# Kernel tuning notes

Measured on AMD Instinct MI355X. Metric: run time of the kernel, lower is better.

Reference implementation:

```python
import jax, jax.numpy as jnp
import numpy as np

D_MODEL = 1024
N_HEADS = 16
D_K = D_MODEL // N_HEADS


def setup_inputs() -> dict:
    key = jax.random.key(0)
    ks = jax.random.split(key, 10)
    B, L = 2, 2048
    s = 1.0 / np.sqrt(D_MODEL)
    inp = {
        "x": jax.random.normal(ks[0], (B, L, D_MODEL), dtype=jnp.float32),
        "bond_influence": jax.random.uniform(ks[1], (B, L, L), dtype=jnp.float32),
        "Wq": jax.random.uniform(ks[2], (D_MODEL, D_MODEL), jnp.float32, -s, s),
        "bq": jax.random.uniform(ks[3], (D_MODEL,), jnp.float32, -s, s),
        "Wk": jax.random.uniform(ks[4], (D_MODEL, D_MODEL), jnp.float32, -s, s),
        "bk": jax.random.uniform(ks[5], (D_MODEL,), jnp.float32, -s, s),
        "Wv": jax.random.uniform(ks[6], (D_MODEL, D_MODEL), jnp.float32, -s, s),
        "bv": jax.random.uniform(ks[7], (D_MODEL,), jnp.float32, -s, s),
        "Wo": jax.random.uniform(ks[8], (D_MODEL, D_MODEL), jnp.float32, -s, s),
        "bo": jax.random.uniform(ks[9], (D_MODEL,), jnp.float32, -s, s),
    }
    return inp


def reference(x, bond_influence, Wq, bq, Wk, bk, Wv, bv, Wo, bo):
    B, L, _ = x.shape
    # QKV projections -> [B, H, L, d_k]
    def proj(W, b):
        return (x @ W + b).reshape(B, L, N_HEADS, D_K).transpose(0, 2, 1, 3)
    Q = proj(Wq, bq)
    K = proj(Wk, bk)
    V = proj(Wv, bv)
    # scores: [B, H, L, L], scaled then modulated by per-batch bond influence
    scores = jnp.einsum('bhqd,bhkd->bhqk', Q, K) / jnp.sqrt(jnp.float32(D_K))
    scores = scores * bond_influence[:, None, :, :]
    attn = jax.nn.softmax(scores, axis=-1)
    out = jnp.einsum('bhqk,bhkd->bhqd', attn, V)  # [B, H, L, d_k]
    out = out.transpose(0, 2, 1, 3).reshape(B, L, D_MODEL)
    return out @ Wo + bo
```

## Files before the change

### kernel.cpp

```cpp
#include <hip/hip_runtime.h>
#include <stdint.h>

typedef unsigned short u16;
typedef __attribute__((ext_vector_type(8))) short bf16x8;
typedef __attribute__((ext_vector_type(4))) float f32x4;

__device__ __forceinline__ u16 f2bf(float f) {
    union { float f; uint32_t u; } v; v.f = f;
    uint32_t u = v.u + 0x7fffu + ((v.u >> 16) & 1u);
    return (u16)(u >> 16);
}
__device__ __forceinline__ float bf2f(u16 s) {
    union { uint32_t u; float f; } v; v.u = ((uint32_t)s) << 16;
    return v.f;
}
__device__ __forceinline__ uint32_t packbf(float a, float b) {
    union { float f; uint32_t u; } ua, ub; ua.f = a; ub.f = b;
    return ((ua.u + 0x8000u) >> 16) | ((ub.u + 0x8000u) & 0xffff0000u);
}

__device__ __forceinline__ void gld16(const void* g, void* l) {
    __builtin_amdgcn_global_load_lds((const __attribute__((address_space(1))) void*)g,
                                     (__attribute__((address_space(3))) void*)l,
                                     16, 0, 0);
}


__global__ void cvt_bf16_kernel(const float* __restrict__ s, u16* __restrict__ d, int n4) {
    int i = blockIdx.x * blockDim.x + threadIdx.x;
    const int stride = gridDim.x * blockDim.x;
    for (; i < n4; i += stride) {
        float4 v = ((const float4*)s)[i];
        ushort4 o;
        o.x = f2bf(v.x); o.y = f2bf(v.y); o.z = f2bf(v.z); o.w = f2bf(v.w);
        ((ushort4*)d)[i] = o;
    }
}

__global__ void transpose_bf16_kernel(const float* __restrict__ src, u16* __restrict__ dst) {
    __shared__ float tile[32][33];
    const int tx = threadIdx.x, ty = threadIdx.y;
    const int bx = blockIdx.x * 32, by = blockIdx.y * 32;
#pragma unroll
    for (int i = ty; i < 32; i += 8)
        tile[i][tx] = src[(size_t)(by + i) * 1024 + bx + tx];
    __syncthreads();
#pragma unroll
    for (int i = ty; i < 32; i += 8)
        dst[(size_t)(bx + i) * 1024 + by + tx] = f2bf(tile[tx][i]);
}


template <int EPI>
__global__ __launch_bounds__(256) void gemm128(
    const u16* __restrict__ A, const u16* __restrict__ Bt,
    const float* __restrict__ bias0, const float* __restrict__ bias1,
    const float* __restrict__ bias2,
    u16* __restrict__ o_q, u16* __restrict__ o_k, u16* __restrict__ o_vt,
    float* __restrict__ o_f)
{
    constexpr int K = 1024;
    __shared__ u16 As[128 * 32];
    __shared__ u16 Bs[128 * 32];
    const int t = threadIdx.x;
    const int lane = t & 63, w = t >> 6;
    const int wm = w >> 1, wn = w & 1;
    const int g = lane >> 4, r = lane & 15;
    const int mbase = blockIdx.y * 128, nbase = blockIdx.x * 128;

    const f32x4 zero4 = {0.f, 0.f, 0.f, 0.f};
    f32x4 acc[4][4];
#pragma unroll
    for (int m = 0; m < 4; ++m)
#pragma unroll
        for (int n = 0; n < 4; ++n) acc[m][n] = zero4;

    for (int k0 = 0; k0 < K; k0 += 32) {
#pragma unroll
        for (int i = 0; i < 2; ++i) {
            const int base = i * 256 + (w << 6);
            const int idx = base + lane;
            const int row = idx >> 2, cc = (idx & 3) << 3;
            gld16(A + (size_t)(mbase + row) * K + k0 + cc, (char*)As + base * 16);
            gld16(Bt + (size_t)(nbase + row) * K + k0 + cc, (char*)Bs + base * 16);
        }
        __syncthreads();

        bf16x8 af[4], bfr[4];
#pragma unroll
        for (int m = 0; m < 4; ++m)
            af[m] = *(const bf16x8*)&As[(wm * 64 + m * 16 + r) * 32 + g * 8];
#pragma unroll
        for (int n = 0; n < 4; ++n)
            bfr[n] = *(const bf16x8*)&Bs[(wn * 64 + n * 16 + r) * 32 + g * 8];
        __builtin_amdgcn_s_setprio(1);
#pragma unroll
        for (int m = 0; m < 4; ++m)
#pragma unroll
            for (int n = 0; n < 4; ++n)
                acc[m][n] = __builtin_amdgcn_mfma_f32_16x16x32_bf16(af[m], bfr[n], acc[m][n], 0, 0, 0);
        __builtin_amdgcn_s_setprio(0);
        __syncthreads();
    }

#pragma unroll
    for (int m = 0; m < 4; ++m) {
#pragma unroll
        for (int n = 0; n < 4; ++n) {
            const int c = nbase + wn * 64 + n * 16 + r;
#pragma unroll
            for (int j = 0; j < 4; ++j) {
                const int rr = mbase + wm * 64 + m * 16 + g * 4 + j;
                const float y = acc[m][n][j];
                if (EPI == 0) {
                    const int which = c >> 10, d = c & 1023;
                    const int b = rr >> 11, l = rr & 2047;
                    const int h = d >> 6, dd = d & 63;
                    const size_t bh = (size_t)(b * 16 + h);
                    if (which == 0) {
                        o_q[(bh * 2048 + l) * 64 + dd] = f2bf((y + bias0[d]) * 0.125f);
                    } else if (which == 1) {
                        o_k[(bh * 2048 + l) * 64 + dd] = f2bf(y + bias1[d]);
                    } else {
                        o_vt[(bh * 64 + dd) * 2048 + l] = f2bf(y + bias2[d]);
                    }
                } else {
                    o_f[(size_t)rr * 1024 + c] = y + bias0[c];
                }
            }
        }
    }
}


__global__ __launch_bounds__(128, 2) void attn_kernel(
    const u16* __restrict__ qb, const u16* __restrict__ kb,
    const u16* __restrict__ vtb, const float* __restrict__ bondf,
    u16* __restrict__ attnout)
{
    __shared__ u16 Ks[2][64 * 64];
    __shared__ u16 Vs[2][64 * 64];
    __shared__ u16 Ps[2][32 * 64];
    const int t = threadIdx.x;
    const int lane = t & 63, w = t >> 6;
    const int g = lane >> 4, r = lane & 15;
    const int sw = r & 7;
    const int flat = blockIdx.x;
    const int wg = (flat & 7) * 128 + (flat >> 3);
    const int bh = wg >> 5, qt = wg & 31;
    const int b = bh >> 4, h = bh & 15;
    const int q0 = qt * 64 + w * 32;
    const size_t kvBase = (size_t)bh * 2048 * 64;
    const size_t bondRow0 = ((size_t)b * 2048 + q0 + r) * 2048;

    bf16x8 aq[2][2];
#pragma unroll
    for (int qf = 0; qf < 2; ++qf)
#pragma unroll
        for (int kz = 0; kz < 2; ++kz)
            aq[qf][kz] = *(const bf16x8*)&qb[kvBase + (size_t)(q0 + qf * 16 + r) * 64 + kz * 32 + g * 8];

    const f32x4 zero4 = {0.f, 0.f, 0.f, 0.f};
    f32x4 o[2][4];
#pragma unroll
    for (int qf = 0; qf < 2; ++qf)
#pragma unroll
        for (int nf = 0; nf < 4; ++nf) o[qf][nf] = zero4;
    float sm[2] = {0.f, 0.f};

#pragma unroll
    for (int i = 0; i < 4; ++i) {
        const int idx = i * 128 + t;
        const int row = idx >> 3, ch = idx & 7;
        const int chg = ch ^ (row & 7);
        gld16(kb + kvBase + (size_t)row * 64 + chg * 8, (char*)&Ks[0][0] + idx * 16);
        gld16(vtb + ((size_t)bh * 64 + row) * 2048 + chg * 8, (char*)&Vs[0][0] + idx * 16);
    }
    float4 bd[2][4], bdn[2][4];
#pragma unroll
    for (int qf = 0; qf < 2; ++qf)
#pragma unroll
        for (int kf = 0; kf < 4; ++kf)
            bd[qf][kf] = *(const float4*)&bondf[bondRow0 + (size_t)qf * 16 * 2048 + kf * 16 + g * 4];
    __syncthreads();

    for (int it = 0; it < 32; ++it) {
        const int cur = it & 1;
        const int kt = it * 64;
        if (it < 31) {
            const int kt2 = kt + 64;
#pragma unroll
            for (int i = 0; i < 4; ++i) {
                const int idx = i * 128 + t;
                const int row = idx >> 3, ch = idx & 7;
                const int chg = ch ^ (row & 7);
                gld16(kb + kvBase + (size_t)(kt2 + row) * 64 + chg * 8, (char*)&Ks[cur ^ 1][0] + idx * 16);
                gld16(vtb + ((size_t)bh * 64 + row) * 2048 + kt2 + chg * 8, (char*)&Vs[cur ^ 1][0] + idx * 16);
            }
#pragma unroll
            for (int qf = 0; qf < 2; ++qf)
#pragma unroll
                for (int kf = 0; kf < 4; ++kf)
                    bdn[qf][kf] = *(const float4*)&bondf[bondRow0 + (size_t)qf * 16 * 2048 + kt2 + kf * 16 + g * 4];
        }

        f32x4 st[2][4];
#pragma unroll
        for (int qf = 0; qf < 2; ++qf)
#pragma unroll
            for (int kf = 0; kf < 4; ++kf) st[qf][kf] = zero4;
        {
            bf16x8 kfr[2][2];
#pragma unroll
            for (int kz = 0; kz < 2; ++kz)
#pragma unroll
                for (int kf = 0; kf < 2; ++kf)
                    kfr[kz][kf] = *(const bf16x8*)((const char*)&Ks[cur][0] +
                                    (kf * 16 + r) * 128 + (((kz * 4 + g) ^ sw) * 16));
            __builtin_amdgcn_s_setprio(1);
#pragma unroll
            for (int kz = 0; kz < 2; ++kz)
#pragma unroll
                for (int qf = 0; qf < 2; ++qf)
#pragma unroll
                    for (int kf = 0; kf < 2; ++kf)
                        st[qf][kf] = __builtin_amdgcn_mfma_f32_16x16x32_bf16(kfr[kz][kf], aq[qf][kz], st[qf][kf], 0, 0, 0);
            __builtin_amdgcn_s_setprio(0);
        }

#pragma unroll
        for (int qf = 0; qf < 2; ++qf)
#pragma unroll
            for (int kf = 0; kf < 2; ++kf) {
                const float p0 = __expf(st[qf][kf][0] * bd[qf][kf].x);
                const float p1 = __expf(st[qf][kf][1] * bd[qf][kf].y);
                const float p2 = __expf(st[qf][kf][2] * bd[qf][kf].z);
                const float p3 = __expf(st[qf][kf][3] * bd[qf][kf].w);
                sm[qf] += (p0 + p1) + (p2 + p3);
                uint2 pk;
                pk.x = packbf(p0, p1);
                pk.y = packbf(p2, p3);
                *(uint2*)((char*)&Ps[w][0] + (qf * 16 + r) * 128 + ((kf * 32 + g * 8) ^ (sw << 4))) = pk;
            }

        {
            bf16x8 kfr[2][2];
#pragma unroll
            for (int kz = 0; kz < 2; ++kz)
#pragma unroll
                for (int kf = 0; kf < 2; ++kf)
                    kfr[kz][kf] = *(const bf16x8*)((const char*)&Ks[cur][0] +
                                    ((kf + 2) * 16 + r) * 128 + (((kz * 4 + g) ^ sw) * 16));
            __builtin_amdgcn_s_setprio(1);
#pragma unroll
            for (int kz = 0; kz < 2; ++kz)
#pragma unroll
                for (int qf = 0; qf < 2; ++qf)
#pragma unroll
                    for (int kf = 0; kf < 2; ++kf)
                        st[qf][kf + 2] = __builtin_amdgcn_mfma_f32_16x16x32_bf16(kfr[kz][kf], aq[qf][kz], st[qf][kf + 2], 0, 0, 0);
            __builtin_amdgcn_s_setprio(0);
        }

        {
            bf16x8 ap[2], bv_[4];
#pragma unroll
            for (int qf = 0; qf < 2; ++qf)
                ap[qf] = *(const bf16x8*)((const char*)&Ps[w][0] +
                            (qf * 16 + r) * 128 + ((g * 16) ^ (sw << 4)));
#pragma unroll
            for (int nf = 0; nf < 4; ++nf)
                bv_[nf] = *(const bf16x8*)((const char*)&Vs[cur][0] +
                            (nf * 16 + r) * 128 + ((g ^ sw) * 16));
            __builtin_amdgcn_s_setprio(1);
#pragma unroll
            for (int qf = 0; qf < 2; ++qf)
#pragma unroll
                for (int nf = 0; nf < 4; ++nf)
                    o[qf][nf] = __builtin_amdgcn_mfma_f32_16x16x32_bf16(ap[qf], bv_[nf], o[qf][nf], 0, 0, 0);
            __builtin_amdgcn_s_setprio(0);
        }

#pragma unroll
        for (int qf = 0; qf < 2; ++qf)
#pragma unroll
            for (int kf = 2; kf < 4; ++kf) {
                const float p0 = __expf(st[qf][kf][0] * bd[qf][kf].x);
                const float p1 = __expf(st[qf][kf][1] * bd[qf][kf].y);
                const float p2 = __expf(st[qf][kf][2] * bd[qf][kf].z);
                const float p3 = __expf(st[qf][kf][3] * bd[qf][kf].w);
                sm[qf] += (p0 + p1) + (p2 + p3);
                uint2 pk;
                pk.x = packbf(p0, p1);
                pk.y = packbf(p2, p3);
                *(uint2*)((char*)&Ps[w][0] + (qf * 16 + r) * 128 + ((kf * 32 + g * 8) ^ (sw << 4))) = pk;
            }

        {
            bf16x8 ap[2], bv_[4];
#pragma unroll
            for (int qf = 0; qf < 2; ++qf)
                ap[qf] = *(const bf16x8*)((const char*)&Ps[w][0] +
                            (qf * 16 + r) * 128 + ((64 + g * 16) ^ (sw << 4)));
#pragma unroll
            for (int nf = 0; nf < 4; ++nf)
                bv_[nf] = *(const bf16x8*)((const char*)&Vs[cur][0] +
                            (nf * 16 + r) * 128 + (((4 + g) ^ sw) * 16));
            __builtin_amdgcn_s_setprio(1);
#pragma unroll
            for (int qf = 0; qf < 2; ++qf)
#pragma unroll
                for (int nf = 0; nf < 4; ++nf)
                    o[qf][nf] = __builtin_amdgcn_mfma_f32_16x16x32_bf16(ap[qf], bv_[nf], o[qf][nf], 0, 0, 0);
            __builtin_amdgcn_s_setprio(0);
        }

        if (it < 31) {
#pragma unroll
            for (int qf = 0; qf < 2; ++qf)
#pragma unroll
                for (int kf = 0; kf < 4; ++kf)
                    bd[qf][kf] = bdn[qf][kf];
        }
        __syncthreads();
    }

#pragma unroll
    for (int qf = 0; qf < 2; ++qf) {
        sm[qf] += __shfl_xor(sm[qf], 16, 64);
        sm[qf] += __shfl_xor(sm[qf], 32, 64);
    }
    float* Lw = (float*)&Ps[w][0];
    if (g == 0) { Lw[r] = sm[0]; Lw[16 + r] = sm[1]; }
    __syncthreads();
    f32x4 lv[2];
    lv[0] = *(const f32x4*)&Lw[g * 4];
    lv[1] = *(const f32x4*)&Lw[16 + g * 4];

#pragma unroll
    for (int qf = 0; qf < 2; ++qf)
#pragma unroll
        for (int j = 0; j < 4; ++j) {
            const float inv = 1.f / lv[qf][j];
            const size_t orow = ((size_t)b * 2048 + q0 + qf * 16 + g * 4 + j) * 1024 + h * 64;
#pragma unroll
            for (int nf = 0; nf < 4; ++nf)
                attnout[orow + nf * 16 + r] = f2bf(o[qf][nf][j] * inv);
        }
}


extern "C" void kernel_launch(void* const* d_in, const int* in_sizes, int n_in,
                              void* d_out, int out_size, void* d_ws, size_t ws_size,
                              hipStream_t stream) {
    (void)in_sizes; (void)n_in; (void)out_size; (void)ws_size;
    const float* x    = (const float*)d_in[0];
    const float* bond = (const float*)d_in[1];
    const float* Wq   = (const float*)d_in[2];
    const float* bq   = (const float*)d_in[3];
    const float* Wk   = (const float*)d_in[4];
    const float* bk   = (const float*)d_in[5];
    const float* Wv   = (const float*)d_in[6];
    const float* bv   = (const float*)d_in[7];
    const float* Wo   = (const float*)d_in[8];
    const float* bo   = (const float*)d_in[9];
    float* out = (float*)d_out;

    char* ws = (char*)d_ws;
    u16* xb      = (u16*)(ws);
    u16* wqkvt   = (u16*)(ws + 8388608);
    u16* wot     = (u16*)(ws + 14680064);
    u16* qb      = (u16*)(ws + 16777216);
    u16* kb_     = (u16*)(ws + 25165824);
    u16* vtb     = (u16*)(ws + 33554432);
    u16* attnout = (u16*)(ws + 58720256);

    dim3 tb(32, 8);
    transpose_bf16_kernel<<<dim3(32, 32), tb, 0, stream>>>(Wq, wqkvt);
    transpose_bf16_kernel<<<dim3(32, 32), tb, 0, stream>>>(Wk, wqkvt + 1024 * 1024);
    transpose_bf16_kernel<<<dim3(32, 32), tb, 0, stream>>>(Wv, wqkvt + 2 * 1024 * 1024);
    transpose_bf16_kernel<<<dim3(32, 32), tb, 0, stream>>>(Wo, wot);
    cvt_bf16_kernel<<<1024, 256, 0, stream>>>(x, xb, 4194304 / 4);

    gemm128<0><<<dim3(24, 32), 256, 0, stream>>>(xb, wqkvt, bq, bk, bv, qb, kb_, vtb, nullptr);
    attn_kernel<<<dim3(1024), 128, 0, stream>>>(qb, kb_, vtb, bond, attnout);
    gemm128<1><<<dim3(8, 32), 256, 0, stream>>>(attnout, wot, bo, nullptr, nullptr,
                                                nullptr, nullptr, nullptr, out);
}
```

Baseline: 171.8 us.

## Keep softmax probabilities in registers via permlane swap instead of LDS round-trip

The attention kernel no longer writes the exponentiated scores to shared memory and reads them back as MFMA A-operands. It repacks them in registers with v_permlane16_swap and permutes the V fragment reads to match the new k ordering. The row-sum broadcast now uses a warp shuffle instead of an LDS write plus __syncthreads. The four weight-transpose launches are also merged into one 3D-grid launch. This cuts LDS traffic, a barrier and launch overhead, but relies on the gfx950 permlane instruction and on the permuted V indexing being correct.

```diff
diff --git a/kernel.cpp b/kernel.cpp
--- a/kernel.cpp
+++ b/kernel.cpp
@@ -10,10 +10,6 @@
     uint32_t u = v.u + 0x7fffu + ((v.u >> 16) & 1u);
     return (u16)(u >> 16);
 }
-__device__ __forceinline__ float bf2f(u16 s) {
-    union { uint32_t u; float f; } v; v.u = ((uint32_t)s) << 16;
-    return v.f;
-}
 __device__ __forceinline__ uint32_t packbf(float a, float b) {
     union { float f; uint32_t u; } ua, ub; ua.f = a; ub.f = b;
     return ((ua.u + 0x8000u) >> 16) | ((ub.u + 0x8000u) & 0xffff0000u);
@@ -23,6 +19,10 @@
     __builtin_amdgcn_global_load_lds((const __attribute__((address_space(1))) void*)g,
                                      (__attribute__((address_space(3))) void*)l,
                                      16, 0, 0);
+}
+
+__device__ __forceinline__ void plswap16(uint32_t& a, uint32_t& b) {
+    asm volatile("v_permlane16_swap_b32 %0, %1" : "+v"(a), "+v"(b));
 }
 
 
@@ -37,8 +37,13 @@
     }
 }
 
-__global__ void transpose_bf16_kernel(const float* __restrict__ src, u16* __restrict__ dst) {
+__global__ void transpose4_bf16_kernel(const float* __restrict__ Wq, const float* __restrict__ Wk,
+                                       const float* __restrict__ Wv, const float* __restrict__ Wo,
+                                       u16* __restrict__ dqkv, u16* __restrict__ dо) {
     __shared__ float tile[32][33];
+    const int z = blockIdx.z;
+    const float* src = (z == 0) ? Wq : (z == 1) ? Wk : (z == 2) ? Wv : Wo;
+    u16* dst = (z < 3) ? (dqkv + (size_t)z * 1024 * 1024) : dо;
     const int tx = threadIdx.x, ty = threadIdx.y;
     const int bx = blockIdx.x * 32, by = blockIdx.y * 32;
 #pragma unroll
@@ -140,11 +145,11 @@
 {
     __shared__ u16 Ks[2][64 * 64];
     __shared__ u16 Vs[2][64 * 64];
-    __shared__ u16 Ps[2][32 * 64];
     const int t = threadIdx.x;
     const int lane = t & 63, w = t >> 6;
     const int g = lane >> 4, r = lane & 15;
     const int sw = r & 7;
+    const int pg = ((g & 1) << 1) | (g >> 1);
     const int flat = blockIdx.x;
     const int wg = (flat & 7) * 128 + (flat >> 3);
     const int bh = wg >> 5, qt = wg & 31;
@@ -205,10 +210,6 @@
         }
 
         f32x4 st[2][4];
-#pragma unroll
-        for (int qf = 0; qf < 2; ++qf)
-#pragma unroll
-            for (int kf = 0; kf < 4; ++kf) st[qf][kf] = zero4;
         {
             bf16x8 kfr[2][2];
 #pragma unroll
@@ -217,6 +218,10 @@
                 for (int kf = 0; kf < 2; ++kf)
                     kfr[kz][kf] = *(const bf16x8*)((const char*)&Ks[cur][0] +
                                     (kf * 16 + r) * 128 + (((kz * 4 + g) ^ sw) * 16));
+#pragma unroll
+            for (int qf = 0; qf < 2; ++qf)
+#pragma unroll
+                for (int kf = 0; kf < 2; ++kf) st[qf][kf] = zero4;
             __builtin_amdgcn_s_setprio(1);
 #pragma unroll
             for (int kz = 0; kz < 2; ++kz)
@@ -228,8 +233,10 @@
             __builtin_amdgcn_s_setprio(0);
         }
 
-#pragma unroll
-        for (int qf = 0; qf < 2; ++qf)
+        bf16x8 ap0[2], ap1[2];
+#pragma unroll
+        for (int qf = 0; qf < 2; ++qf) {
+            uint32_t pkl[2], pkh[2];
 #pragma unroll
             for (int kf = 0; kf < 2; ++kf) {
                 const float p0 = __expf(st[qf][kf][0] * bd[qf][kf].x);
@@ -237,11 +244,15 @@
                 const float p2 = __expf(st[qf][kf][2] * bd[qf][kf].z);
                 const float p3 = __expf(st[qf][kf][3] * bd[qf][kf].w);
                 sm[qf] += (p0 + p1) + (p2 + p3);
-                uint2 pk;
-                pk.x = packbf(p0, p1);
-                pk.y = packbf(p2, p3);
-                *(uint2*)((char*)&Ps[w][0] + (qf * 16 + r) * 128 + ((kf * 32 + g * 8) ^ (sw << 4))) = pk;
+                pkl[kf] = packbf(p0, p1);
+                pkh[kf] = packbf(p2, p3);
             }
+            plswap16(pkl[0], pkl[1]);
+            plswap16(pkh[0], pkh[1]);
+            union { uint32_t u[4]; bf16x8 v; } a;
+            a.u[0] = pkl[0]; a.u[1] = pkh[0]; a.u[2] = pkl[1]; a.u[3] = pkh[1];
+            ap0[qf] = a.v;
+        }
 
         {
             bf16x8 kfr[2][2];
@@ -251,6 +262,10 @@
                 for (int kf = 0; kf < 2; ++kf)
                     kfr[kz][kf] = *(const bf16x8*)((const char*)&Ks[cur][0] +
                                     ((kf + 2) * 16 + r) * 128 + (((kz * 4 + g) ^ sw) * 16));
+#pragma unroll
+            for (int qf = 0; qf < 2; ++qf)
+#pragma unroll
+                for (int kf = 0; kf < 2; ++kf) st[qf][kf + 2] = zero4;
             __builtin_amdgcn_s_setprio(1);
 #pragma unroll
             for (int kz = 0; kz < 2; ++kz)
@@ -263,55 +278,52 @@
         }
 
         {
-            bf16x8 ap[2], bv_[4];
-#pragma unroll
-            for (int qf = 0; qf < 2; ++qf)
-                ap[qf] = *(const bf16x8*)((const char*)&Ps[w][0] +
-                            (qf * 16 + r) * 128 + ((g * 16) ^ (sw << 4)));
+            bf16x8 bv_[4];
 #pragma unroll
             for (int nf = 0; nf < 4; ++nf)
                 bv_[nf] = *(const bf16x8*)((const char*)&Vs[cur][0] +
-                            (nf * 16 + r) * 128 + ((g ^ sw) * 16));
+                            (nf * 16 + r) * 128 + ((pg ^ sw) * 16));
             __builtin_amdgcn_s_setprio(1);
 #pragma unroll
             for (int qf = 0; qf < 2; ++qf)
 #pragma unroll
                 for (int nf = 0; nf < 4; ++nf)
-                    o[qf][nf] = __builtin_amdgcn_mfma_f32_16x16x32_bf16(ap[qf], bv_[nf], o[qf][nf], 0, 0, 0);
+                    o[qf][nf] = __builtin_amdgcn_mfma_f32_16x16x32_bf16(ap0[qf], bv_[nf], o[qf][nf], 0, 0, 0);
             __builtin_amdgcn_s_setprio(0);
         }
 
 #pragma unroll
-        for (int qf = 0; qf < 2; ++qf)
-#pragma unroll
-            for (int kf = 2; kf < 4; ++kf) {
-                const float p0 = __expf(st[qf][kf][0] * bd[qf][kf].x);
-                const float p1 = __expf(st[qf][kf][1] * bd[qf][kf].y);
-                const float p2 = __expf(st[qf][kf][2] * bd[qf][kf].z);
-                const float p3 = __expf(st[qf][kf][3] * bd[qf][kf].w);
+        for (int qf = 0; qf < 2; ++qf) {
+            uint32_t pkl[2], pkh[2];
+#pragma unroll
+            for (int kf = 0; kf < 2; ++kf) {
+                const float p0 = __expf(st[qf][kf + 2][0] * bd[qf][kf + 2].x);
+                const float p1 = __expf(st[qf][kf + 2][1] * bd[qf][kf + 2].y);
+                const float p2 = __expf(st[qf][kf + 2][2] * bd[qf][kf + 2].z);
+                const float p3 = __expf(st[qf][kf + 2][3] * bd[qf][kf + 2].w);
                 sm[qf] += (p0 + p1) + (p2 + p3);
-                uint2 pk;
-                pk.x = packbf(p0, p1);
-                pk.y = packbf(p2, p3);
-                *(uint2*)((char*)&Ps[w][0] + (qf * 16 + r) * 128 + ((kf * 32 + g * 8) ^ (sw << 4))) = pk;
+                pkl[kf] = packbf(p0, p1);
+                pkh[kf] = packbf(p2, p3);
             }
+            plswap16(pkl[0], pkl[1]);
+            plswap16(pkh[0], pkh[1]);
+            union { uint32_t u[4]; bf16x8 v; } a;
+            a.u[0] = pkl[0]; a.u[1] = pkh[0]; a.u[2] = pkl[1]; a.u[3] = pkh[1];
+            ap1[qf] = a.v;
+        }
 
         {
-            bf16x8 ap[2], bv_[4];
-#pragma unroll
-            for (int qf = 0; qf < 2; ++qf)
-                ap[qf] = *(const bf16x8*)((const char*)&Ps[w][0] +
-                            (qf * 16 + r) * 128 + ((64 + g * 16) ^ (sw << 4)));
+            bf16x8 bv_[4];
 #pragma unroll
             for (int nf = 0; nf < 4; ++nf)
                 bv_[nf] = *(const bf16x8*)((const char*)&Vs[cur][0] +
-                            (nf * 16 + r) * 128 + (((4 + g) ^ sw) * 16));
+                            (nf * 16 + r) * 128 + (((4 + pg) ^ sw) * 16));
             __builtin_amdgcn_s_setprio(1);
 #pragma unroll
             for (int qf = 0; qf < 2; ++qf)
 #pragma unroll
                 for (int nf = 0; nf < 4; ++nf)
-                    o[qf][nf] = __builtin_amdgcn_mfma_f32_16x16x32_bf16(ap[qf], bv_[nf], o[qf][nf], 0, 0, 0);
+                    o[qf][nf] = __builtin_amdgcn_mfma_f32_16x16x32_bf16(ap1[qf], bv_[nf], o[qf][nf], 0, 0, 0);
             __builtin_amdgcn_s_setprio(0);
         }
 
@@ -330,18 +342,11 @@
         sm[qf] += __shfl_xor(sm[qf], 16, 64);
         sm[qf] += __shfl_xor(sm[qf], 32, 64);
     }
-    float* Lw = (float*)&Ps[w][0];
-    if (g == 0) { Lw[r] = sm[0]; Lw[16 + r] = sm[1]; }
-    __syncthreads();
-    f32x4 lv[2];
-    lv[0] = *(const f32x4*)&Lw[g * 4];
-    lv[1] = *(const f32x4*)&Lw[16 + g * 4];
-
 #pragma unroll
     for (int qf = 0; qf < 2; ++qf)
 #pragma unroll
         for (int j = 0; j < 4; ++j) {
-            const float inv = 1.f / lv[qf][j];
+            const float inv = 1.f / __shfl(sm[qf], g * 4 + j, 16);
             const size_t orow = ((size_t)b * 2048 + q0 + qf * 16 + g * 4 + j) * 1024 + h * 64;
 #pragma unroll
             for (int nf = 0; nf < 4; ++nf)
@@ -376,10 +381,7 @@
     u16* attnout = (u16*)(ws + 58720256);
 
     dim3 tb(32, 8);
-    transpose_bf16_kernel<<<dim3(32, 32), tb, 0, stream>>>(Wq, wqkvt);
-    transpose_bf16_kernel<<<dim3(32, 32), tb, 0, stream>>>(Wk, wqkvt + 1024 * 1024);
-    transpose_bf16_kernel<<<dim3(32, 32), tb, 0, stream>>>(Wv, wqkvt + 2 * 1024 * 1024);
-    transpose_bf16_kernel<<<dim3(32, 32), tb, 0, stream>>>(Wo, wot);
+    transpose4_bf16_kernel<<<dim3(32, 32, 4), tb, 0, stream>>>(Wq, Wk, Wv, Wo, wqkvt, wot);
     cvt_bf16_kernel<<<1024, 256, 0, stream>>>(x, xb, 4194304 / 4);
 
     gemm128<0><<<dim3(24, 32), 256, 0, stream>>>(xb, wqkvt, bq, bk, bv, qb, kb_, vtb, nullptr);
```

After: 164.3 us. -4.3%, faster.
